# Kernel optimization log

Measured on AMD Instinct MI355X. Metric: run time of the kernel, lower is better.

## Reference

```python
import jax, jax.numpy as jnp
import numpy as np

HEAD_DIM = 128
BAND_BITS = (5, 4, 4, 3)
N_BANDS = len(BAND_BITS)
BAND = HEAD_DIM // N_BANDS  # 32
FP16_MAX = 65504.0


def _hadamard(n):
    H = np.array([[1.0]], dtype=np.float32)
    while H.shape[0] < n:
        H = np.block([[H, H], [H, -H]])
    return H


def _mobius_perm(n):
    # Mobius function mu(i) for i = 1..n via sieve
    mu = np.ones(n + 1, dtype=np.int64)
    is_prime = np.ones(n + 1, dtype=bool)
    for p in range(2, n + 1):
        if is_prime[p]:
            is_prime[2 * p::p] = False
            mu[p::p] *= -1
            sq = p * p
            if sq <= n:
                mu[sq::sq] = 0
    # stable reorder of the 0..n-1 coordinates by descending mu(i+1)
    perm = np.argsort(-mu[1:n + 1], kind='stable').astype(np.int32)
    inv = np.argsort(perm).astype(np.int32)
    return perm, inv

_H = jnp.asarray(_hadamard(HEAD_DIM))            # [128,128], symmetric, H@H = 128*I
_PERM, _INV_PERM = (jnp.asarray(p) for p in _mobius_perm(HEAD_DIM))


def _banded_quant_dequant(z):
    # z: [N, HEAD_DIM] in WHT+Mobius space. Per-row, per-band symmetric quantization.
    zb = z.reshape(-1, N_BANDS, BAND)                       # [N, 4, 32]
    qmax = jnp.asarray([2 ** (b - 1) - 1 for b in BAND_BITS], jnp.float32)  # [4]
    amax = jnp.max(jnp.abs(zb), axis=-1)                    # [N, 4]
    scale = jnp.where(amax > 0, amax / qmax, 1.0)           # [N, 4]
    q = jnp.clip(jnp.round(zb / scale[..., None]), -qmax[:, None], qmax[:, None])
    return (q * scale[..., None]).reshape(-1, HEAD_DIM)


def setup_inputs() -> dict:
    key = jax.random.key(0)
    k1, k2 = jax.random.split(key)
    x = jax.random.normal(k1, (2, 512, 5120), dtype=jnp.float32)
    W = jax.random.normal(k2, (5120, 5120), dtype=jnp.float32) * 0.02
    b = jnp.zeros((5120,), dtype=jnp.float32)
    return {"x": x, "W": W, "b": b}


def reference(x, W, b):
    # cache-miss path: linear projection (result = cross_attn proj of T5 context)
    y = jnp.einsum('bld,ed->ble', x, W) + b                 # [B, L, 5120]
    orig_shape = y.shape
    yf = y.reshape(-1, HEAD_DIM)                            # [B*L*n_heads, 128]
    # put(): WHT -> Mobius reorder -> banded quantize
    z = yf @ _H                                             # unnormalized WHT
    z = z[:, _PERM]
    z = _banded_quant_dequant(z)
    # get(): un-reorder -> inverse WHT (WHT then /head_dim) -> clamp/nan_to_num
    z = z[:, _INV_PERM]
    r = (z @ _H) / HEAD_DIM
    r = jnp.clip(r, -FP16_MAX, FP16_MAX)
    r = jnp.nan_to_num(r, nan=0.0)
    return r.reshape(orig_shape)
```

## Files before the change

kernel.cpp:

```cpp
#include <hip/hip_runtime.h>
#include <math.h>

#define HEAD 128
typedef _Float16 f16;
typedef _Float16 f16x8 __attribute__((ext_vector_type(8)));
typedef _Float16 f16x4 __attribute__((ext_vector_type(4)));
typedef float f32x4 __attribute__((ext_vector_type(4)));

constexpr int mu_of(int n) {
  int m = n, cnt = 0;
  for (int p = 2; p * p <= m; ++p) {
    if (m % p == 0) {
      m /= p; ++cnt;
      if (m % p == 0) return 0;
    }
  }
  if (m > 1) ++cnt;
  return (cnt & 1) ? -1 : 1;
}
constexpr int key_of(int idx) {
  int mu = mu_of(idx + 1);
  return mu == 1 ? 0 : (mu == 0 ? 1 : 2);
}
struct Tbl {
  int band[HEAD];
  float qm[HEAD];
};
constexpr Tbl make_tbl() {
  Tbl t{};
  constexpr float qv[4] = {15.f, 7.f, 7.f, 3.f};
  for (int p = 0; p < HEAD; ++p) {
    int kp = key_of(p);
    int rank = 0;
    for (int j = 0; j < HEAD; ++j) {
      int kj = key_of(j);
      if (kj < kp || (kj == kp && j < p)) ++rank;
    }
    t.band[p] = rank >> 5;
    t.qm[p] = qv[rank >> 5];
  }
  return t;
}
__constant__ Tbl g_tbl = make_tbl();

__global__ __launch_bounds__(256) void split64_2(
    const float* __restrict__ x, const float* __restrict__ W,
    f16* __restrict__ xh, f16* __restrict__ xl,
    f16* __restrict__ wh, f16* __restrict__ wl, int n4x, int n4tot) {
  int i = blockIdx.x * blockDim.x + threadIdx.x;
  if (i >= n4tot) return;
  const float* s;
  f16 *h, *l;
  int j;
  if (i < n4x) {
    s = x; h = xh; l = xl; j = i;
  } else {
    s = W; h = wh; l = wl; j = i - n4x;
  }
  float4 v = ((const float4*)s)[j];
  v.x *= 64.f; v.y *= 64.f; v.z *= 64.f; v.w *= 64.f;
  f16 hx = (f16)v.x, hy = (f16)v.y, hz = (f16)v.z, hw = (f16)v.w;
  f16 lx = (f16)(v.x - (float)hx);
  f16 ly = (f16)(v.y - (float)hy);
  f16 lz = (f16)(v.z - (float)hz);
  f16 lw = (f16)(v.w - (float)hw);
  f16x4 hv = {hx, hy, hz, hw};
  f16x4 lv = {lx, ly, lz, lw};
  *(f16x4*)(h + 4 * (size_t)j) = hv;
  *(f16x4*)(l + 4 * (size_t)j) = lv;
}

__device__ __forceinline__ void dma16(const f16* g, f16* l) {
  __builtin_amdgcn_global_load_lds(
      (const __attribute__((address_space(1))) unsigned int*)g,
      (__attribute__((address_space(3))) unsigned int*)l, 16, 0, 0);
}

__global__ __launch_bounds__(256) void gemm_f16split_sk(
    const f16* __restrict__ Ah, const f16* __restrict__ Al,
    const f16* __restrict__ Bh, const f16* __restrict__ Bl,
    const float* __restrict__ bias, float* __restrict__ C0,
    float* __restrict__ Cp, int M, int N, int K, int nsplit) {
  __shared__ f16 sAh[4096];
  __shared__ f16 sAl[4096];
  __shared__ f16 sBh[4096];
  __shared__ f16 sBl[4096];

  const int tid = threadIdx.x;
  const int lane = tid & 63;
  const int wave = tid >> 6;
  const int wr = wave >> 1;
  const int wc = wave & 1;

  const int nbm = M >> 7;
  const int nbn = N >> 7;
  const int tiles = nbm * nbn;
  const int nwg = gridDim.x;
  int wgid = blockIdx.x;
  if ((nwg & 7) == 0) {
    const int cpx = nwg >> 3;
    wgid = (wgid & 7) * cpx + (wgid >> 3);
  }
  const int split = wgid / tiles;
  const int tix = wgid % tiles;
  const int mb = tix % nbm;
  const int nb = tix / nbm;
  const int m0 = mb * 128;
  const int n0 = nb * 128;
  const int Ks = K / nsplit;
  const int k_beg = split * Ks;
  const int k_end = k_beg + Ks;

  const int rsel = wave * 16 + (lane & 15);
  const int ksel = (lane >> 4) * 8;
  const f16* pAh = Ah + (size_t)(m0 + rsel) * K + ksel;
  const f16* pAl = Al + (size_t)(m0 + rsel) * K + ksel;
  const f16* pBh = Bh + (size_t)(n0 + rsel) * K + ksel;
  const f16* pBl = Bl + (size_t)(n0 + rsel) * K + ksel;
  const size_t r64 = (size_t)64 * K;

  f16* dA0h = sAh + wave * 512;
  f16* dA1h = sAh + 2048 + wave * 512;
  f16* dA0l = sAl + wave * 512;
  f16* dA1l = sAl + 2048 + wave * 512;
  f16* dB0h = sBh + wave * 512;
  f16* dB1h = sBh + 2048 + wave * 512;
  f16* dB0l = sBl + wave * 512;
  f16* dB1l = sBl + 2048 + wave * 512;

  f32x4 acc[4][4];
#pragma unroll
  for (int i = 0; i < 4; ++i)
#pragma unroll
    for (int j = 0; j < 4; ++j) acc[i][j] = (f32x4){0.f, 0.f, 0.f, 0.f};

  auto stage = [&](int k0) {
    dma16(pAh + k0, dA0h);
    dma16(pAh + k0 + r64, dA1h);
    dma16(pAl + k0, dA0l);
    dma16(pAl + k0 + r64, dA1l);
    dma16(pBh + k0, dB0h);
    dma16(pBh + k0 + r64, dB1h);
    dma16(pBl + k0, dB0l);
    dma16(pBl + k0 + r64, dB1l);
  };

  stage(k_beg);

  const int lb = lane * 8;
  const int ca = wr * 4 * 512;
  const int cb = wc * 4 * 512;

  for (int k0 = k_beg; k0 < k_end; k0 += 32) {
    __syncthreads();

    f16x8 ah[4], al[4], bh[4], bl[4];
#pragma unroll
    for (int i = 0; i < 4; ++i) {
      ah[i] = *(const f16x8*)&sAh[ca + i * 512 + lb];
      al[i] = *(const f16x8*)&sAl[ca + i * 512 + lb];
      bh[i] = *(const f16x8*)&sBh[cb + i * 512 + lb];
      bl[i] = *(const f16x8*)&sBl[cb + i * 512 + lb];
    }
    __syncthreads();

    if (k0 + 32 < k_end) stage(k0 + 32);

    __builtin_amdgcn_s_setprio(1);
#pragma unroll
    for (int i = 0; i < 4; ++i)
#pragma unroll
      for (int j = 0; j < 4; ++j) {
        acc[i][j] = __builtin_amdgcn_mfma_f32_16x16x32_f16(ah[i], bh[j], acc[i][j], 0, 0, 0);
        acc[i][j] = __builtin_amdgcn_mfma_f32_16x16x32_f16(al[i], bh[j], acc[i][j], 0, 0, 0);
        acc[i][j] = __builtin_amdgcn_mfma_f32_16x16x32_f16(ah[i], bl[j], acc[i][j], 0, 0, 0);
      }
    __builtin_amdgcn_s_setprio(0);
  }

  const float inv = 1.f / 4096.f;
  const int frow = lane & 15;
  const int kq = lane >> 4;
  const size_t MN = (size_t)M * N;
  float* dst = (split == 0) ? C0 : (Cp + (size_t)(split - 1) * MN);
#pragma unroll
  for (int j = 0; j < 4; ++j) {
    const int col = n0 + wc * 64 + j * 16 + frow;
    const float bv = (split == 0) ? bias[col] : 0.f;
#pragma unroll
    for (int i = 0; i < 4; ++i) {
#pragma unroll
      for (int r = 0; r < 4; ++r) {
        const int row = m0 + wr * 64 + i * 16 + kq * 4 + r;
        dst[(size_t)row * N + col] = acc[i][j][r] * inv + bv;
      }
    }
  }
}

#define BM 128
#define BN 64
#define BKK 8
#define TM 8
#define TN 4

__global__ __launch_bounds__(256) void sgemm_nt(
    const float* __restrict__ A, const float* __restrict__ B,
    const float* __restrict__ bias, float* __restrict__ C,
    int M, int N, int K) {
  __shared__ float As[BKK][BM];
  __shared__ float Bs[BKK][BN];

  const int tid = threadIdx.x;
  const int tn = tid & 15;
  const int tm = tid >> 4;
  const int bx = blockIdx.x;
  const int by = blockIdx.y;

  const float* Ab = A + (size_t)by * BM * K;
  const float* Bb = B + (size_t)bx * BN * K;

  const int ar = tid >> 1;
  const int ak = (tid & 1) * 4;

  float acc[TM][TN];
#pragma unroll
  for (int i = 0; i < TM; ++i)
#pragma unroll
    for (int j = 0; j < TN; ++j) acc[i][j] = 0.f;

  for (int k0 = 0; k0 < K; k0 += BKK) {
    float4 av = *(const float4*)(Ab + (size_t)ar * K + k0 + ak);
    float4 bv = make_float4(0.f, 0.f, 0.f, 0.f);
    if (tid < 128) bv = *(const float4*)(Bb + (size_t)ar * K + k0 + ak);

    __syncthreads();
    As[ak + 0][ar] = av.x;
    As[ak + 1][ar] = av.y;
    As[ak + 2][ar] = av.z;
    As[ak + 3][ar] = av.w;
    if (tid < 128) {
      Bs[ak + 0][ar] = bv.x;
      Bs[ak + 1][ar] = bv.y;
      Bs[ak + 2][ar] = bv.z;
      Bs[ak + 3][ar] = bv.w;
    }
    __syncthreads();

#pragma unroll
    for (int kk = 0; kk < BKK; ++kk) {
      float a[TM], b[TN];
#pragma unroll
      for (int i = 0; i < TM; ++i) a[i] = As[kk][tm * TM + i];
#pragma unroll
      for (int j = 0; j < TN; ++j) b[j] = Bs[kk][tn * TN + j];
#pragma unroll
      for (int i = 0; i < TM; ++i)
#pragma unroll
        for (int j = 0; j < TN; ++j) acc[i][j] += a[i] * b[j];
    }
  }

  const int row0 = by * BM + tm * TM;
  const int col0 = bx * BN + tn * TN;
  float bj[TN];
#pragma unroll
  for (int j = 0; j < TN; ++j) bj[j] = bias[col0 + j];
#pragma unroll
  for (int i = 0; i < TM; ++i) {
    float4 v = make_float4(acc[i][0] + bj[0], acc[i][1] + bj[1],
                           acc[i][2] + bj[2], acc[i][3] + bj[3]);
    *(float4*)(C + (size_t)(row0 + i) * N + col0) = v;
  }
}

__device__ inline void fwht2(float& e0, float& e1, int lane) {
  float a = e0 + e1;
  float b = e0 - e1;
  e0 = a;
  e1 = b;
#pragma unroll
  for (int s = 1; s <= 32; s <<= 1) {
    float p0 = __shfl_xor(e0, s);
    float p1 = __shfl_xor(e1, s);
    bool up = (lane & s) != 0;
    e0 = up ? (p0 - e0) : (e0 + p0);
    e1 = up ? (p1 - e1) : (e1 + p1);
  }
}

__global__ __launch_bounds__(256) void hadq(const float* __restrict__ Y,
                                            const float* __restrict__ P,
                                            int npart, float* __restrict__ O,
                                            int nrows) {
  const int lane = threadIdx.x & 63;
  const int wave = (blockIdx.x * (blockDim.x >> 6)) + (threadIdx.x >> 6);
  const int nwaves = gridDim.x * (blockDim.x >> 6);

  const int b0 = g_tbl.band[lane];
  const int b1 = g_tbl.band[lane + 64];
  const float qm0 = g_tbl.qm[lane];
  const float qm1 = g_tbl.qm[lane + 64];
  const size_t MN = (size_t)nrows * HEAD;

  for (int row = wave; row < nrows; row += nwaves) {
    const float* y = Y + (size_t)row * HEAD;
    float e0 = y[lane];
    float e1 = y[lane + 64];
    for (int p = 0; p < npart; ++p) {
      const float* pp = P + (size_t)p * MN + (size_t)row * HEAD;
      e0 += pp[lane];
      e1 += pp[lane + 64];
    }

    fwht2(e0, e1, lane);

    float f0 = fabsf(e0), f1 = fabsf(e1);
    float ab0 = fmaxf(b0 == 0 ? f0 : 0.f, b1 == 0 ? f1 : 0.f);
    float ab1 = fmaxf(b0 == 1 ? f0 : 0.f, b1 == 1 ? f1 : 0.f);
    float ab2 = fmaxf(b0 == 2 ? f0 : 0.f, b1 == 2 ? f1 : 0.f);
    float ab3 = fmaxf(b0 == 3 ? f0 : 0.f, b1 == 3 ? f1 : 0.f);
#pragma unroll
    for (int s = 32; s >= 1; s >>= 1) {
      ab0 = fmaxf(ab0, __shfl_xor(ab0, s));
      ab1 = fmaxf(ab1, __shfl_xor(ab1, s));
      ab2 = fmaxf(ab2, __shfl_xor(ab2, s));
      ab3 = fmaxf(ab3, __shfl_xor(ab3, s));
    }
    float am0 = b0 == 0 ? ab0 : (b0 == 1 ? ab1 : (b0 == 2 ? ab2 : ab3));
    float am1 = b1 == 0 ? ab0 : (b1 == 1 ? ab1 : (b1 == 2 ? ab2 : ab3));

    float s0 = am0 > 0.f ? am0 / qm0 : 1.0f;
    float s1 = am1 > 0.f ? am1 / qm1 : 1.0f;

    float q0 = fminf(fmaxf(rintf(e0 / s0), -qm0), qm0);
    float q1 = fminf(fmaxf(rintf(e1 / s1), -qm1), qm1);
    e0 = q0 * s0;
    e1 = q1 * s1;

    fwht2(e0, e1, lane);
    float r0 = e0 * 0.0078125f;
    float r1 = e1 * 0.0078125f;
    if (r0 != r0) r0 = 0.f;
    if (r1 != r1) r1 = 0.f;
    r0 = fminf(fmaxf(r0, -65504.f), 65504.f);
    r1 = fminf(fmaxf(r1, -65504.f), 65504.f);

    float* o = O + (size_t)row * HEAD;
    o[lane] = r0;
    o[lane + 64] = r1;
  }
}

extern "C" void kernel_launch(void* const* d_in, const int* in_sizes, int n_in,
                              void* d_out, int out_size, void* d_ws, size_t ws_size,
                              hipStream_t stream) {
  const float* x = (const float*)d_in[0];
  const float* W = (const float*)d_in[1];
  const float* b = (const float*)d_in[2];
  float* out = (float*)d_out;

  const int N = in_sizes[2];
  const int K = N;
  const int M = in_sizes[0] / K;

  const size_t MK = (size_t)M * K;
  const size_t NK = (size_t)N * K;
  const size_t MN = (size_t)M * N;
  const size_t need = (MK + NK) * 2 * sizeof(f16);

  const int nrows = out_size / HEAD;

  if (ws_size >= need && (M % 128) == 0 && (N % 128) == 0 && (K % 32) == 0) {
    f16* xh = (f16*)d_ws;
    f16* xl = xh + MK;
    f16* wh = xl + MK;
    f16* wl = wh + NK;
    float* Cp = (float*)((char*)d_ws + need);

    int nsplit = 1;
    if (ws_size >= need + 3 * MN * sizeof(float) && (K % 128) == 0)
      nsplit = 4;
    else if (ws_size >= need + 1 * MN * sizeof(float) && (K % 64) == 0)
      nsplit = 2;

    const int n4x = (int)(MK / 4);
    const int n4tot = (int)((MK + NK) / 4);
    split64_2<<<(n4tot + 255) / 256, 256, 0, stream>>>(x, W, xh, xl, wh, wl,
                                                       n4x, n4tot);

    const int nwg = (M / 128) * (N / 128) * nsplit;
    gemm_f16split_sk<<<nwg, 256, 0, stream>>>(xh, xl, wh, wl, b, out, Cp, M,
                                              N, K, nsplit);

    hadq<<<512, 256, 0, stream>>>(out, Cp, nsplit - 1, out, nrows);
  } else {
    dim3 grid(N / BN, M / BM);
    sgemm_nt<<<grid, 256, 0, stream>>>(x, W, b, out, M, N, K);
    hadq<<<512, 256, 0, stream>>>(out, (const float*)out, 0, out, nrows);
  }
}
```

Baseline: 421.2 us.

## Double-buffer LDS in split-K f16 GEMM with two tiles in flight

The GEMM's shared-memory staging goes from one buffer to two, and the next-next K tile is prefetched while the current one is consumed. Explicit vmcnt/lgkmcnt waits with raw s_barrier replace __syncthreads, so global-to-LDS DMA overlaps the MFMA work. LDS use doubles to 64KB per block, which may reduce occupancy. The fast-path guard now requires K divisible by 64.

```diff
diff --git a/kernel.cpp b/kernel.cpp
--- a/kernel.cpp
+++ b/kernel.cpp
@@ -76,15 +76,15 @@
       (__attribute__((address_space(3))) unsigned int*)l, 16, 0, 0);
 }
 
-__global__ __launch_bounds__(256) void gemm_f16split_sk(
+__global__ __launch_bounds__(256) void gemm_f16split_db(
     const f16* __restrict__ Ah, const f16* __restrict__ Al,
     const f16* __restrict__ Bh, const f16* __restrict__ Bl,
     const float* __restrict__ bias, float* __restrict__ C0,
     float* __restrict__ Cp, int M, int N, int K, int nsplit) {
-  __shared__ f16 sAh[4096];
-  __shared__ f16 sAl[4096];
-  __shared__ f16 sBh[4096];
-  __shared__ f16 sBl[4096];
+  __shared__ f16 sAh[2][4096];
+  __shared__ f16 sAl[2][4096];
+  __shared__ f16 sBh[2][4096];
+  __shared__ f16 sBl[2][4096];
 
   const int tid = threadIdx.x;
   const int lane = tid & 63;
@@ -109,7 +109,6 @@
   const int n0 = nb * 128;
   const int Ks = K / nsplit;
   const int k_beg = split * Ks;
-  const int k_end = k_beg + Ks;
 
   const int rsel = wave * 16 + (lane & 15);
   const int ksel = (lane >> 4) * 8;
@@ -119,52 +118,54 @@
   const f16* pBl = Bl + (size_t)(n0 + rsel) * K + ksel;
   const size_t r64 = (size_t)64 * K;
 
-  f16* dA0h = sAh + wave * 512;
-  f16* dA1h = sAh + 2048 + wave * 512;
-  f16* dA0l = sAl + wave * 512;
-  f16* dA1l = sAl + 2048 + wave * 512;
-  f16* dB0h = sBh + wave * 512;
-  f16* dB1h = sBh + 2048 + wave * 512;
-  f16* dB0l = sBl + wave * 512;
-  f16* dB1l = sBl + 2048 + wave * 512;
-
   f32x4 acc[4][4];
 #pragma unroll
   for (int i = 0; i < 4; ++i)
 #pragma unroll
     for (int j = 0; j < 4; ++j) acc[i][j] = (f32x4){0.f, 0.f, 0.f, 0.f};
 
-  auto stage = [&](int k0) {
-    dma16(pAh + k0, dA0h);
-    dma16(pAh + k0 + r64, dA1h);
-    dma16(pAl + k0, dA0l);
-    dma16(pAl + k0 + r64, dA1l);
-    dma16(pBh + k0, dB0h);
-    dma16(pBh + k0 + r64, dB1h);
-    dma16(pBl + k0, dB0l);
-    dma16(pBl + k0 + r64, dB1l);
+  auto stage = [&](int k0, int b) {
+    dma16(pAh + k0, &sAh[b][wave * 512]);
+    dma16(pAh + k0 + r64, &sAh[b][2048 + wave * 512]);
+    dma16(pAl + k0, &sAl[b][wave * 512]);
+    dma16(pAl + k0 + r64, &sAl[b][2048 + wave * 512]);
+    dma16(pBh + k0, &sBh[b][wave * 512]);
+    dma16(pBh + k0 + r64, &sBh[b][2048 + wave * 512]);
+    dma16(pBl + k0, &sBl[b][wave * 512]);
+    dma16(pBl + k0 + r64, &sBl[b][2048 + wave * 512]);
   };
 
-  stage(k_beg);
+  const int nt = Ks >> 5;
+  stage(k_beg, 0);
+  if (nt > 1) stage(k_beg + 32, 1);
 
   const int lb = lane * 8;
   const int ca = wr * 4 * 512;
   const int cb = wc * 4 * 512;
 
-  for (int k0 = k_beg; k0 < k_end; k0 += 32) {
-    __syncthreads();
-
+  for (int t = 0; t < nt; ++t) {
+    if (t + 1 < nt) {
+      asm volatile("s_waitcnt vmcnt(8)" ::: "memory");
+    } else {
+      asm volatile("s_waitcnt vmcnt(0)" ::: "memory");
+    }
+    __builtin_amdgcn_sched_barrier(0);
+    __builtin_amdgcn_s_barrier();
+
+    const int b = t & 1;
     f16x8 ah[4], al[4], bh[4], bl[4];
 #pragma unroll
     for (int i = 0; i < 4; ++i) {
-      ah[i] = *(const f16x8*)&sAh[ca + i * 512 + lb];
-      al[i] = *(const f16x8*)&sAl[ca + i * 512 + lb];
-      bh[i] = *(const f16x8*)&sBh[cb + i * 512 + lb];
-      bl[i] = *(const f16x8*)&sBl[cb + i * 512 + lb];
-    }
-    __syncthreads();
-
-    if (k0 + 32 < k_end) stage(k0 + 32);
+      ah[i] = *(const f16x8*)&sAh[b][ca + i * 512 + lb];
+      al[i] = *(const f16x8*)&sAl[b][ca + i * 512 + lb];
+      bh[i] = *(const f16x8*)&sBh[b][cb + i * 512 + lb];
+      bl[i] = *(const f16x8*)&sBl[b][cb + i * 512 + lb];
+    }
+    asm volatile("s_waitcnt lgkmcnt(0)" ::: "memory");
+    __builtin_amdgcn_sched_barrier(0);
+    __builtin_amdgcn_s_barrier();
+
+    if (t + 2 < nt) stage(k_beg + (t + 2) * 32, b);
 
     __builtin_amdgcn_s_setprio(1);
 #pragma unroll
@@ -371,7 +372,7 @@
 
   const int nrows = out_size / HEAD;
 
-  if (ws_size >= need && (M % 128) == 0 && (N % 128) == 0 && (K % 32) == 0) {
+  if (ws_size >= need && (M % 128) == 0 && (N % 128) == 0 && (K % 64) == 0) {
     f16* xh = (f16*)d_ws;
     f16* xl = xh + MK;
     f16* wh = xl + MK;
@@ -390,7 +391,7 @@
                                                        n4x, n4tot);
 
     const int nwg = (M / 128) * (N / 128) * nsplit;
-    gemm_f16split_sk<<<nwg, 256, 0, stream>>>(xh, xl, wh, wl, b, out, Cp, M,
+    gemm_f16split_db<<<nwg, 256, 0, stream>>>(xh, xl, wh, wl, b, out, Cp, M,
                                               N, K, nsplit);
 
     hadq<<<512, 256, 0, stream>>>(out, Cp, nsplit - 1, out, nrows);
```

Result: no change. 427.0 us (+1.4%).
